# Optimization experiments

Hardware: AMD Instinct MI355X
Metric: run time of the kernel (lower is better)

## Reference

```python
import jax, jax.numpy as jnp
import numpy as np

B, L, D, H, DFF = 4, 2048, 1024, 16, 4096
DH = D // H
INF = 1e12


def setup_inputs() -> dict:
    key = jax.random.key(0)
    ks = jax.random.split(key, 20)
    s = lambda fan_in: 1.0 / np.sqrt(fan_in)
    inp = {
        'x': jax.random.normal(ks[0], (B, L, D), jnp.float32),
        'mask': jax.random.bernoulli(ks[1], 0.1, (B, 1, 1, L)),
        'wq': jax.random.normal(ks[2], (D, D), jnp.float32) * s(D),
        'bq': jnp.zeros((D,), jnp.float32),
        'wk': jax.random.normal(ks[3], (D, D), jnp.float32) * s(D),
        'bk': jnp.zeros((D,), jnp.float32),
        'wv': jax.random.normal(ks[4], (D, D), jnp.float32) * s(D),
        'bv': jnp.zeros((D,), jnp.float32),
        'wo': jax.random.normal(ks[5], (D, D), jnp.float32) * s(D),
        'bo': jnp.zeros((D,), jnp.float32),
        'w1': jax.random.normal(ks[6], (D, DFF), jnp.float32) * s(D),
        'b1': jnp.zeros((DFF,), jnp.float32),
        'w2': jax.random.normal(ks[7], (DFF, D), jnp.float32) * s(DFF),
        'b2': jnp.zeros((D,), jnp.float32),
        'g1': jnp.ones((D,), jnp.float32),
        'beta1': jnp.zeros((D,), jnp.float32),
        'g2': jnp.ones((D,), jnp.float32),
        'beta2': jnp.zeros((D,), jnp.float32),
    }
    return inp


def _layernorm(x, g, b, eps=1e-5):
    mu = jnp.mean(x, axis=-1, keepdims=True)
    var = jnp.mean(jnp.square(x - mu), axis=-1, keepdims=True)
    return (x - mu) * jax.lax.rsqrt(var + eps) * g + b


def reference(x, mask, wq, bq, wk, bk, wv, bv, wo, bo, w1, b1, w2, b2, g1, beta1, g2, beta2):
    # --- self attention ---
    def split_heads(t):  # [B,L,D] -> [B,H,L,DH]
        return t.reshape(B, L, H, DH).transpose(0, 2, 1, 3)

    Q = split_heads(x @ wq + bq)
    K = split_heads(x @ wk + bk)
    V = split_heads(x @ wv + bv)

    dots = jnp.einsum('bhqd,bhkd->bhqk', Q, K) / np.sqrt(DH)  # [B,H,L,L]
    dots = jnp.where(mask, -INF, dots)
    attn = jax.nn.softmax(dots, axis=-1)
    out = jnp.einsum('bhqk,bhkd->bhqd', attn, V)
    out = out.transpose(0, 2, 1, 3).reshape(B, L, D)
    out = out @ wo + bo

    x = _layernorm(x + out, g1, beta1)

    # --- feed forward ---
    h = jax.nn.relu(x @ w1 + b1)
    ff = h @ w2 + b2
    x = _layernorm(x + ff, g2, beta2)
    return x
```

## Files before the change

kernel.cpp:

```cpp
#include <hip/hip_runtime.h>
#include <hip/hip_bf16.h>

#define B_   4
#define L_   2048
#define D_   1024
#define H_   16
#define DH_  64
#define DFF_ 4096
#define M_   (B_ * L_)

typedef __attribute__((ext_vector_type(8))) short bf16x8;
typedef __attribute__((ext_vector_type(4))) float f32x4;

#define GLOAD16(gp, lp)                                                       \
  __builtin_amdgcn_global_load_lds(                                           \
      (const __attribute__((address_space(1))) unsigned int*)(gp),            \
      (__attribute__((address_space(3))) unsigned int*)(lp), 16, 0, 0)

#if __has_builtin(__builtin_amdgcn_exp2f)
#define EXP2F(x) __builtin_amdgcn_exp2f(x)
#else
#define EXP2F(x) exp2f(x)
#endif

__device__ __forceinline__ float bf2f(unsigned short u) {
  return __uint_as_float(((unsigned)u) << 16);
}

__global__ void prep_all(const float4* __restrict__ x4,
                         ushort4* __restrict__ xb4,
                         const unsigned int* __restrict__ mraw,
                         float* __restrict__ maskf,
                         const float* __restrict__ bq,
                         const float* __restrict__ bk,
                         const float* __restrict__ bv,
                         float* __restrict__ biasc) {
  const int id = blockIdx.x;
  if (id < 8192) {
    const int i = id * 256 + threadIdx.x;
    float4 v = x4[i];
    __hip_bfloat16 a = __float2bfloat16(v.x);
    __hip_bfloat16 b = __float2bfloat16(v.y);
    __hip_bfloat16 c = __float2bfloat16(v.z);
    __hip_bfloat16 d = __float2bfloat16(v.w);
    ushort4 o;
    o.x = *reinterpret_cast<unsigned short*>(&a);
    o.y = *reinterpret_cast<unsigned short*>(&b);
    o.z = *reinterpret_cast<unsigned short*>(&c);
    o.w = *reinterpret_cast<unsigned short*>(&d);
    xb4[i] = o;
    return;
  }
  __shared__ int flags[2];
  if (threadIdx.x < 2) flags[threadIdx.x] = 0;
  __syncthreads();
  int nf32 = 0, n01 = 0;
  for (int i = threadIdx.x; i < 2048; i += 256) {
    unsigned w = mraw[i];
    if (w != 0u && w != 0x3f800000u) nf32 = 1;
    if (w > 1u) n01 = 1;
  }
  if (nf32) atomicOr(&flags[0], 1);
  if (n01)  atomicOr(&flags[1], 1);
  __syncthreads();
  const int mode = (!flags[0]) ? 0 : ((!flags[1]) ? 1 : 2);
  const int mi = (id - 8192) * 256 + threadIdx.x;
  if (mi < B_ * L_) {
    bool mk;
    if (mode == 0)      mk = reinterpret_cast<const float*>(mraw)[mi] != 0.f;
    else if (mode == 1) mk = reinterpret_cast<const int*>(mraw)[mi] != 0;
    else                mk = reinterpret_cast<const unsigned char*>(mraw)[mi] != 0;
    maskf[mi] = mk ? -1e12f : -32.0f;
  }
  if (id == 8192) {
#pragma unroll
    for (int j = 0; j < 4; ++j) {
      const int c = j * 256 + threadIdx.x;
      biasc[c] = bq[c];
      biasc[D_ + c] = bk[c];
      biasc[2 * D_ + c] = bv[c];
    }
  }
}

__global__ void transpose_cvt_all(
    const float* __restrict__ wq, const float* __restrict__ wk,
    const float* __restrict__ wv, const float* __restrict__ wo,
    const float* __restrict__ w1, const float* __restrict__ w2,
    __hip_bfloat16* __restrict__ WQT, __hip_bfloat16* __restrict__ WKT,
    __hip_bfloat16* __restrict__ WVT, __hip_bfloat16* __restrict__ WOT,
    __hip_bfloat16* __restrict__ W1T, __hip_bfloat16* __restrict__ W2T) {
  __shared__ float t[32][33];
  const int id = blockIdx.x;
  const float* W;
  __hip_bfloat16* Wt;
  int K, N, rem;
  if (id < 4096) {
    const int which = id >> 10;
    W  = which == 0 ? wq : which == 1 ? wk : which == 2 ? wv : wo;
    Wt = which == 0 ? WQT : which == 1 ? WKT : which == 2 ? WVT : WOT;
    K = D_; N = D_; rem = id & 1023;
  } else if (id < 8192) {
    W = w1; Wt = W1T; K = D_; N = DFF_; rem = id - 4096;
  } else {
    W = w2; Wt = W2T; K = DFF_; N = D_; rem = id - 8192;
  }
  const int ntx = N >> 5;
  const int n0 = (rem % ntx) * 32, k0 = (rem / ntx) * 32;
  const int tx = threadIdx.x, ty = threadIdx.y;
#pragma unroll
  for (int i = 0; i < 4; ++i)
    t[ty + i * 8][tx] = W[(size_t)(k0 + ty + i * 8) * N + n0 + tx];
  __syncthreads();
#pragma unroll
  for (int i = 0; i < 4; ++i)
    Wt[(size_t)(n0 + ty + i * 8) * K + k0 + tx] =
        __float2bfloat16(t[tx][ty + i * 8]);
}

__global__ void transpose_v(const __hip_bfloat16* __restrict__ Vin,
                            __hip_bfloat16* __restrict__ Vt) {
  __shared__ __hip_bfloat16 t[32][33];
  const int l0 = blockIdx.x * 32, d0 = blockIdx.y * 32, b = blockIdx.z;
  const int tx = threadIdx.x, ty = threadIdx.y;
#pragma unroll
  for (int i = 0; i < 4; ++i)
    t[ty + i * 8][tx] = Vin[(size_t)(b * L_ + l0 + ty + i * 8) * D_ + d0 + tx];
  __syncthreads();
#pragma unroll
  for (int i = 0; i < 4; ++i) {
    int d = d0 + ty + i * 8;
    Vt[(size_t)(b * D_ + d) * L_ + l0 + tx] = t[tx][ty + i * 8];
  }
}

#define STAGE8(matptr, stride, ldsbase, tile, kh, rowbase)                    \
  {                                                                           \
    _Pragma("unroll")                                                         \
    for (int j_ = 0; j_ < 2; ++j_) {                                          \
      const int s_ = j_ * 512 + tid;                                          \
      const int row_ = s_ >> 2;                                               \
      const int q_ = (s_ & 3) ^ ((row_ >> 1) & 3);                            \
      GLOAD16(&matptr[(size_t)((rowbase) + row_) * (stride) + (tile) * 64 +   \
                      (kh) * 32 + q_ * 8],                                    \
              (ldsbase) + (j_ * 512 + (w << 6)) * 16);                        \
    }                                                                         \
  }

#define PHASE8(bufoff, rh, ks, dovm, ...)                                     \
  {                                                                           \
    if ((rh) == 0) {                                                          \
      _Pragma("unroll")                                                       \
      for (int j = 0; j < 4; ++j) {                                           \
        const int br = wn * 64 + j * 16 + r16;                                \
        bfr[j] = *reinterpret_cast<const bf16x8*>(                            \
            ldsB + (bufoff) + (ks) * 16384 + br * 64 +                        \
            ((hi * 16) ^ (((br >> 1) & 3) << 4)));                            \
      }                                                                       \
    }                                                                         \
    bf16x8 af[4];                                                             \
    _Pragma("unroll")                                                         \
    for (int i = 0; i < 4; ++i) {                                             \
      const int ar = wm * 128 + (rh) * 64 + i * 16 + r16;                     \
      af[i] = *reinterpret_cast<const bf16x8*>(                               \
          ldsA + (bufoff) + (ks) * 16384 + ar * 64 +                          \
          ((hi * 16) ^ (((ar >> 1) & 3) << 4)));                              \
    }                                                                         \
    __VA_ARGS__;                                                              \
    __builtin_amdgcn_s_barrier();                                             \
    asm volatile("s_waitcnt lgkmcnt(0)" ::: "memory");                        \
    __builtin_amdgcn_sched_barrier(0);                                        \
    __builtin_amdgcn_s_setprio(1);                                            \
    _Pragma("unroll")                                                         \
    for (int i = 0; i < 4; ++i)                                               \
      _Pragma("unroll")                                                       \
      for (int j = 0; j < 4; ++j)                                             \
        acc[(rh) * 4 + i][j] = __builtin_amdgcn_mfma_f32_16x16x32_bf16(       \
            af[i], bfr[j], acc[(rh) * 4 + i][j], 0, 0, 0);                    \
    __builtin_amdgcn_s_setprio(0);                                            \
    if (dovm) {                                                               \
      asm volatile("s_waitcnt vmcnt(4)" ::: "memory");                        \
      __builtin_amdgcn_sched_barrier(0);                                      \
    }                                                                         \
    __builtin_amdgcn_s_barrier();                                             \
  }

template <int EP>
__global__ __launch_bounds__(512, 1) void gemm8(
    const __hip_bfloat16* __restrict__ A, const __hip_bfloat16* __restrict__ Bt,
    const float* __restrict__ bias, void* __restrict__ out,
    int M, int N, int K, int lda, int ldb) {
  __shared__ __align__(16) char lds8[131072];
  char* const ldsA = lds8;
  char* const ldsB = lds8 + 65536;

  const int tid = threadIdx.x;
  const int lane = tid & 63;
  const int w = tid >> 6;
  const int wm = w >> 2;
  const int wn = w & 3;
  const int r16 = lane & 15;
  const int hi = lane >> 4;

  const int nwg = gridDim.x;
  const int orig = blockIdx.x;
  const int swz = (orig & 7) * (nwg >> 3) + (orig >> 3);

  int bm, bn, kh = 0;
  const __hip_bfloat16* Ap = A;
  const __hip_bfloat16* Bp = Bt;
  if (EP == 4) {
    kh = swz & 1;
    const int rest = swz >> 1;
    bm = (rest & 31) * 256;
    bn = (rest >> 5) * 256;
    Ap += (size_t)kh * K;
    Bp += (size_t)kh * K;
  } else {
    bm = (swz & 31) * 256;
    bn = (swz >> 5) * 256;
  }

  f32x4 acc[8][4];
#pragma unroll
  for (int i = 0; i < 8; ++i)
#pragma unroll
    for (int j = 0; j < 4; ++j) acc[i][j] = (f32x4){0.f, 0.f, 0.f, 0.f};
  bf16x8 bfr[4];

  const int nkt = K >> 6;
  const int nit = nkt >> 1;

  STAGE8(Ap, lda, ldsA, 0, 0, bm);
  STAGE8(Bp, ldb, ldsB, 0, 0, bn);
  STAGE8(Ap, lda, ldsA + 16384, 0, 1, bm);
  STAGE8(Bp, ldb, ldsB + 16384, 0, 1, bn);
  STAGE8(Ap, lda, ldsA + 32768, 1, 0, bm);
  STAGE8(Bp, ldb, ldsB + 32768, 1, 0, bn);
  asm volatile("s_waitcnt vmcnt(4)" ::: "memory");
  __builtin_amdgcn_sched_barrier(0);
  __builtin_amdgcn_s_barrier();

  for (int it = 0; it < nit; ++it) {
    const int kt = it * 2;
    const bool hn = (it + 1) < nit;
    PHASE8(0, 0, 0, 0, STAGE8(Ap, lda, ldsA + 49152, kt + 1, 1, bm));
    PHASE8(0, 1, 0, 0, STAGE8(Bp, ldb, ldsB + 49152, kt + 1, 1, bn));
    PHASE8(0, 0, 1, 0, if (hn) STAGE8(Ap, lda, ldsA, kt + 2, 0, bm));
    PHASE8(0, 1, 1, 1, if (hn) STAGE8(Bp, ldb, ldsB, kt + 2, 0, bn));
    PHASE8(32768, 0, 0, 0, if (hn) STAGE8(Ap, lda, ldsA + 16384, kt + 2, 1, bm));
    PHASE8(32768, 1, 0, 0, if (hn) STAGE8(Bp, ldb, ldsB + 16384, kt + 2, 1, bn));
    PHASE8(32768, 0, 1, 0, if (hn) STAGE8(Ap, lda, ldsA + 32768, kt + 3, 0, bm));
    PHASE8(32768, 1, 1, 1, if (hn) STAGE8(Bp, ldb, ldsB + 32768, kt + 3, 0, bn));
  }

#pragma unroll
  for (int ri = 0; ri < 8; ++ri) {
#pragma unroll
    for (int j = 0; j < 4; ++j) {
      const int col = bn + wn * 64 + j * 16 + r16;
      const float bv = (EP == 4) ? 0.f : bias[col];
#pragma unroll
      for (int r = 0; r < 4; ++r) {
        const int row = bm + wm * 128 + ri * 16 + hi * 4 + r;
        const float v = acc[ri][j][r] + bv;
        if (EP == 1) {
          ((__hip_bfloat16*)out)[(size_t)row * N + col] =
              __float2bfloat16(v > 0.f ? v : 0.f);
        } else if (EP == 3) {
          __hip_bfloat16* outp =
              (__hip_bfloat16*)out + (size_t)(col >> 10) * (M_ * D_);
          outp[(size_t)row * 1024 + (col & 1023)] = __float2bfloat16(v);
        } else {
          __hip_bfloat16* outp =
              (__hip_bfloat16*)out + (size_t)kh * ((size_t)M * N);
          outp[(size_t)row * N + col] = __float2bfloat16(v);
        }
      }
    }
  }
}

template <int EP>
__global__ __launch_bounds__(256) void gemm_bt(
    const __hip_bfloat16* __restrict__ A, const __hip_bfloat16* __restrict__ Bt,
    const float* __restrict__ bias, const float* __restrict__ res,
    void* __restrict__ out, int M, int N, int K) {
  __shared__ __align__(16) char As[128 * 64];
  __shared__ __align__(16) char Bs[128 * 64];
  const int tid = threadIdx.x;
  const int lane = tid & 63;
  const int w = tid >> 6;
  const int wm = w >> 1, wn = w & 1;
  const int bm = blockIdx.x * 128;
  const int bn = blockIdx.y * 128;
  const int r16 = lane & 15;
  const int hi = lane >> 4;

  f32x4 acc[4][4];
#pragma unroll
  for (int m = 0; m < 4; ++m)
#pragma unroll
    for (int n = 0; n < 4; ++n) acc[m][n] = (f32x4){0.f, 0.f, 0.f, 0.f};

  for (int k0 = 0; k0 < K; k0 += 32) {
    __syncthreads();
#pragma unroll
    for (int c = 0; c < 2; ++c) {
      const int seg = c * 256 + tid;
      const int row = seg >> 2;
      const int csl = (seg & 3) ^ (row & 3);
      GLOAD16(&A[(size_t)(bm + row) * K + k0 + csl * 8],
              As + (c * 256 + w * 64) * 16);
      GLOAD16(&Bt[(size_t)(bn + row) * K + k0 + csl * 8],
              Bs + (c * 256 + w * 64) * 16);
    }
    __syncthreads();

    bf16x8 af[4], bfr[4];
#pragma unroll
    for (int m = 0; m < 4; ++m) {
      const int arow = wm * 64 + m * 16 + r16;
      af[m] = *reinterpret_cast<const bf16x8*>(
          As + arow * 64 + ((hi * 16) ^ ((arow & 3) << 4)));
    }
#pragma unroll
    for (int n = 0; n < 4; ++n) {
      const int brow = wn * 64 + n * 16 + r16;
      bfr[n] = *reinterpret_cast<const bf16x8*>(
          Bs + brow * 64 + ((hi * 16) ^ ((brow & 3) << 4)));
    }
#pragma unroll
    for (int m = 0; m < 4; ++m)
#pragma unroll
      for (int n = 0; n < 4; ++n)
        acc[m][n] = __builtin_amdgcn_mfma_f32_16x16x32_bf16(af[m], bfr[n],
                                                            acc[m][n], 0, 0, 0);
  }

  const int rg = hi * 4;
#pragma unroll
  for (int m = 0; m < 4; ++m) {
#pragma unroll
    for (int n = 0; n < 4; ++n) {
      const int col = bn + wn * 64 + n * 16 + r16;
      const float bv = bias[col];
#pragma unroll
      for (int r = 0; r < 4; ++r) {
        const int row = bm + wm * 64 + m * 16 + rg + r;
        const size_t idx = (size_t)row * N + col;
        float v = acc[m][n][r] + bv;
        if (EP == 0) {
          ((__hip_bfloat16*)out)[idx] = __float2bfloat16(v);
        } else {
          ((float*)out)[idx] = v + res[idx];
        }
      }
    }
  }
}

__global__ __launch_bounds__(256) void attn_kernel(
    const __hip_bfloat16* __restrict__ Qg, const __hip_bfloat16* __restrict__ Kg,
    const __hip_bfloat16* __restrict__ VTg,
    const float* __restrict__ maskf,
    __hip_bfloat16* __restrict__ Og) {
  __shared__ __align__(16) char Kl[64 * 128];
  __shared__ __align__(16) char Vl[64 * 128];
  __shared__ __align__(16) char Pl[4][32 * 128];
  __shared__ float maskb[64];

  const int tid = threadIdx.x;
  const int lane = tid & 63;
  const int w = tid >> 6;
  const int hi = lane >> 4;
  const int r16 = lane & 15;
  const int swzk = (r16 & 7) << 4;

  const int nwg = gridDim.x;
  const int orig = blockIdx.x;
  const int swb = (orig & 7) * (nwg >> 3) + (orig >> 3);
  const int qb = swb & 15;
  const int bh = swb >> 4;
  const int b = bh >> 4;
  const int h = bh & 15;
  const int qbase = qb * 128 + w * 32;

  const float C = 0.18033688011112042f;
  const short ob = (short)0x3f80;
  const bf16x8 vone = {ob, ob, ob, ob, ob, ob, ob, ob};

  bf16x8 qf[2][2];
#pragma unroll
  for (int m = 0; m < 2; ++m)
#pragma unroll
    for (int ks = 0; ks < 2; ++ks)
      qf[m][ks] = *reinterpret_cast<const bf16x8*>(
          &Qg[(size_t)(b * L_ + qbase + m * 16 + r16) * D_ + h * DH_ +
              ks * 32 + hi * 8]);

  f32x4 o[2][4];
  f32x4 oden[2];
#pragma unroll
  for (int m = 0; m < 2; ++m) {
    oden[m] = (f32x4){0.f, 0.f, 0.f, 0.f};
#pragma unroll
    for (int nd = 0; nd < 4; ++nd) o[m][nd] = (f32x4){0.f, 0.f, 0.f, 0.f};
  }

  char* const Plw = Pl[w];

  for (int kv0 = 0; kv0 < L_; kv0 += 64) {
    __syncthreads();
#pragma unroll
    for (int c = 0; c < 2; ++c) {
      const int seg = c * 256 + tid;
      const int row = seg >> 3;
      const int csl = (seg & 7) ^ (row & 7);
      GLOAD16(&Kg[(size_t)(b * L_ + kv0 + row) * D_ + h * DH_ + csl * 8],
              Kl + (c * 256 + w * 64) * 16);
      GLOAD16(&VTg[(size_t)(b * D_ + h * DH_ + row) * L_ + kv0 + csl * 8],
              Vl + (c * 256 + w * 64) * 16);
    }
    if (tid < 64) maskb[tid] = maskf[(size_t)b * L_ + kv0 + tid];
    __syncthreads();

    f32x4 sacc[2][4];
#pragma unroll
    for (int m = 0; m < 2; ++m)
#pragma unroll
      for (int n = 0; n < 4; ++n) sacc[m][n] = (f32x4){0.f, 0.f, 0.f, 0.f};
    __builtin_amdgcn_s_setprio(1);
#pragma unroll
    for (int n = 0; n < 4; ++n) {
      const int krow = n * 16 + r16;
#pragma unroll
      for (int ks = 0; ks < 2; ++ks) {
        const bf16x8 kf = *reinterpret_cast<const bf16x8*>(
            Kl + krow * 128 + ((ks * 64 + hi * 16) ^ swzk));
#pragma unroll
        for (int m = 0; m < 2; ++m)
          sacc[m][n] = __builtin_amdgcn_mfma_f32_16x16x32_bf16(
              kf, qf[m][ks], sacc[m][n], 0, 0, 0);
      }
    }
    __builtin_amdgcn_s_setprio(0);

    float4 mv[4];
#pragma unroll
    for (int n = 0; n < 4; ++n)
      mv[n] = *reinterpret_cast<const float4*>(&maskb[n * 16 + hi * 4]);
#pragma unroll
    for (int m = 0; m < 2; ++m) {
      const int prow = m * 16 + r16;
#pragma unroll
      for (int n = 0; n < 4; ++n) {
        const float e0 = EXP2F(fmaf(sacc[m][n][0], C, mv[n].x));
        const float e1 = EXP2F(fmaf(sacc[m][n][1], C, mv[n].y));
        const float e2 = EXP2F(fmaf(sacc[m][n][2], C, mv[n].z));
        const float e3 = EXP2F(fmaf(sacc[m][n][3], C, mv[n].w));
        union { unsigned long long u; unsigned short us[4]; } pk;
        __hip_bfloat16 t0 = __float2bfloat16(e0);
        __hip_bfloat16 t1 = __float2bfloat16(e1);
        __hip_bfloat16 t2 = __float2bfloat16(e2);
        __hip_bfloat16 t3 = __float2bfloat16(e3);
        pk.us[0] = *reinterpret_cast<unsigned short*>(&t0);
        pk.us[1] = *reinterpret_cast<unsigned short*>(&t1);
        pk.us[2] = *reinterpret_cast<unsigned short*>(&t2);
        pk.us[3] = *reinterpret_cast<unsigned short*>(&t3);
        *reinterpret_cast<unsigned long long*>(
            Plw + prow * 128 + ((n * 32 + hi * 8) ^ swzk)) = pk.u;
      }
    }

    bf16x8 pa[2][2];
#pragma unroll
    for (int m = 0; m < 2; ++m)
#pragma unroll
      for (int ks = 0; ks < 2; ++ks)
        pa[m][ks] = *reinterpret_cast<const bf16x8*>(
            Plw + (m * 16 + r16) * 128 + ((ks * 64 + hi * 16) ^ swzk));
    __builtin_amdgcn_s_setprio(1);
#pragma unroll
    for (int m = 0; m < 2; ++m)
#pragma unroll
      for (int ks = 0; ks < 2; ++ks)
        oden[m] = __builtin_amdgcn_mfma_f32_16x16x32_bf16(pa[m][ks], vone,
                                                          oden[m], 0, 0, 0);
#pragma unroll
    for (int nd = 0; nd < 4; ++nd) {
      const int vrow = nd * 16 + r16;
#pragma unroll
      for (int ks = 0; ks < 2; ++ks) {
        const bf16x8 vb = *reinterpret_cast<const bf16x8*>(
            Vl + vrow * 128 + ((ks * 64 + hi * 16) ^ swzk));
#pragma unroll
        for (int m = 0; m < 2; ++m)
          o[m][nd] = __builtin_amdgcn_mfma_f32_16x16x32_bf16(pa[m][ks], vb,
                                                             o[m][nd], 0, 0, 0);
      }
    }
    __builtin_amdgcn_s_setprio(0);
  }

#pragma unroll
  for (int m = 0; m < 2; ++m) {
#pragma unroll
    for (int r = 0; r < 4; ++r) {
      const float ir = 1.f / oden[m][r];
      const int q = qbase + m * 16 + hi * 4 + r;
#pragma unroll
      for (int nd = 0; nd < 4; ++nd)
        Og[(size_t)(b * L_ + q) * D_ + h * DH_ + nd * 16 + r16] =
            __float2bfloat16(o[m][nd][r] * ir);
    }
  }
}

__global__ __launch_bounds__(256) void layernorm_kernel(
    const float* __restrict__ in, const float* __restrict__ g,
    const float* __restrict__ be, float* __restrict__ outf,
    __hip_bfloat16* __restrict__ outb) {
  const int row = blockIdx.x;
  const int tid = threadIdx.x;
  const float4 v = reinterpret_cast<const float4*>(in + (size_t)row * D_)[tid];
  float s = v.x + v.y + v.z + v.w;
  float ss = v.x * v.x + v.y * v.y + v.z * v.z + v.w * v.w;
#pragma unroll
  for (int off = 1; off < 64; off <<= 1) {
    s += __shfl_xor(s, off, 64);
    ss += __shfl_xor(ss, off, 64);
  }
  __shared__ float red[8];
  const int w = tid >> 6, lane = tid & 63;
  if (lane == 0) { red[w] = s; red[4 + w] = ss; }
  __syncthreads();
  s = red[0] + red[1] + red[2] + red[3];
  ss = red[4] + red[5] + red[6] + red[7];
  const float mu = s * (1.f / D_);
  const float rs = rsqrtf(ss * (1.f / D_) - mu * mu + 1e-5f);
  const float4 gv = reinterpret_cast<const float4*>(g)[tid];
  const float4 bv = reinterpret_cast<const float4*>(be)[tid];
  float4 ov;
  ov.x = (v.x - mu) * rs * gv.x + bv.x;
  ov.y = (v.y - mu) * rs * gv.y + bv.y;
  ov.z = (v.z - mu) * rs * gv.z + bv.z;
  ov.w = (v.w - mu) * rs * gv.w + bv.w;
  reinterpret_cast<float4*>(outf + (size_t)row * D_)[tid] = ov;
  if (outb) {
    __hip_bfloat16 t[4] = {__float2bfloat16(ov.x), __float2bfloat16(ov.y),
                           __float2bfloat16(ov.z), __float2bfloat16(ov.w)};
    *reinterpret_cast<uint2*>(&outb[(size_t)row * D_ + tid * 4]) =
        *reinterpret_cast<const uint2*>(t);
  }
}

__global__ __launch_bounds__(256) void ln_addres(
    const __hip_bfloat16* __restrict__ OP, const float* __restrict__ x,
    const float* __restrict__ g, const float* __restrict__ be,
    float* __restrict__ outf, __hip_bfloat16* __restrict__ outb) {
  const int row = blockIdx.x;
  const int tid = threadIdx.x;
  const ushort4 a4 = reinterpret_cast<const ushort4*>(OP + (size_t)row * D_)[tid];
  const float4 xr = reinterpret_cast<const float4*>(x + (size_t)row * D_)[tid];
  float4 v;
  v.x = bf2f(a4.x) + xr.x;
  v.y = bf2f(a4.y) + xr.y;
  v.z = bf2f(a4.z) + xr.z;
  v.w = bf2f(a4.w) + xr.w;
  float s = v.x + v.y + v.z + v.w;
  float ss = v.x * v.x + v.y * v.y + v.z * v.z + v.w * v.w;
#pragma unroll
  for (int off = 1; off < 64; off <<= 1) {
    s += __shfl_xor(s, off, 64);
    ss += __shfl_xor(ss, off, 64);
  }
  __shared__ float red[8];
  const int w = tid >> 6, lane = tid & 63;
  if (lane == 0) { red[w] = s; red[4 + w] = ss; }
  __syncthreads();
  s = red[0] + red[1] + red[2] + red[3];
  ss = red[4] + red[5] + red[6] + red[7];
  const float mu = s * (1.f / D_);
  const float rs = rsqrtf(ss * (1.f / D_) - mu * mu + 1e-5f);
  const float4 gv = reinterpret_cast<const float4*>(g)[tid];
  const float4 bv = reinterpret_cast<const float4*>(be)[tid];
  float4 ov;
  ov.x = (v.x - mu) * rs * gv.x + bv.x;
  ov.y = (v.y - mu) * rs * gv.y + bv.y;
  ov.z = (v.z - mu) * rs * gv.z + bv.z;
  ov.w = (v.w - mu) * rs * gv.w + bv.w;
  reinterpret_cast<float4*>(outf + (size_t)row * D_)[tid] = ov;
  __hip_bfloat16 t[4] = {__float2bfloat16(ov.x), __float2bfloat16(ov.y),
                         __float2bfloat16(ov.z), __float2bfloat16(ov.w)};
  *reinterpret_cast<uint2*>(&outb[(size_t)row * D_ + tid * 4]) =
      *reinterpret_cast<const uint2*>(t);
}

__global__ __launch_bounds__(256) void ln_addres_sk(
    const __hip_bfloat16* __restrict__ P0, const __hip_bfloat16* __restrict__ P1,
    const float* __restrict__ x, const float* __restrict__ bo,
    const float* __restrict__ g, const float* __restrict__ be,
    float* __restrict__ outf, __hip_bfloat16* __restrict__ outb) {
  const int row = blockIdx.x;
  const int tid = threadIdx.x;
  const ushort4 a4 = reinterpret_cast<const ushort4*>(P0 + (size_t)row * D_)[tid];
  const ushort4 b4 = reinterpret_cast<const ushort4*>(P1 + (size_t)row * D_)[tid];
  const float4 xr = reinterpret_cast<const float4*>(x + (size_t)row * D_)[tid];
  const float4 bb = reinterpret_cast<const float4*>(bo)[tid];
  float4 v;
  v.x = bf2f(a4.x) + bf2f(b4.x) + xr.x + bb.x;
  v.y = bf2f(a4.y) + bf2f(b4.y) + xr.y + bb.y;
  v.z = bf2f(a4.z) + bf2f(b4.z) + xr.z + bb.z;
  v.w = bf2f(a4.w) + bf2f(b4.w) + xr.w + bb.w;
  float s = v.x + v.y + v.z + v.w;
  float ss = v.x * v.x + v.y * v.y + v.z * v.z + v.w * v.w;
#pragma unroll
  for (int off = 1; off < 64; off <<= 1) {
    s += __shfl_xor(s, off, 64);
    ss += __shfl_xor(ss, off, 64);
  }
  __shared__ float red[8];
  const int w = tid >> 6, lane = tid & 63;
  if (lane == 0) { red[w] = s; red[4 + w] = ss; }
  __syncthreads();
  s = red[0] + red[1] + red[2] + red[3];
  ss = red[4] + red[5] + red[6] + red[7];
  const float mu = s * (1.f / D_);
  const float rs = rsqrtf(ss * (1.f / D_) - mu * mu + 1e-5f);
  const float4 gv = reinterpret_cast<const float4*>(g)[tid];
  const float4 bv = reinterpret_cast<const float4*>(be)[tid];
  float4 ov;
  ov.x = (v.x - mu) * rs * gv.x + bv.x;
  ov.y = (v.y - mu) * rs * gv.y + bv.y;
  ov.z = (v.z - mu) * rs * gv.z + bv.z;
  ov.w = (v.w - mu) * rs * gv.w + bv.w;
  reinterpret_cast<float4*>(outf + (size_t)row * D_)[tid] = ov;
  __hip_bfloat16 t[4] = {__float2bfloat16(ov.x), __float2bfloat16(ov.y),
                         __float2bfloat16(ov.z), __float2bfloat16(ov.w)};
  *reinterpret_cast<uint2*>(&outb[(size_t)row * D_ + tid * 4]) =
      *reinterpret_cast<const uint2*>(t);
}

__global__ __launch_bounds__(256) void combine_ln2(
    const __hip_bfloat16* __restrict__ P0, const __hip_bfloat16* __restrict__ P1,
    const float* __restrict__ res, const float* __restrict__ b2,
    const float* __restrict__ g, const float* __restrict__ be,
    float* __restrict__ out) {
  const int row = blockIdx.x;
  const int tid = threadIdx.x;
  const ushort4 a4 =
      reinterpret_cast<const ushort4*>(P0 + (size_t)row * D_)[tid];
  const ushort4 b4 =
      reinterpret_cast<const ushort4*>(P1 + (size_t)row * D_)[tid];
  const float4 rr = reinterpret_cast<const float4*>(res + (size_t)row * D_)[tid];
  const float4 bb = reinterpret_cast<const float4*>(b2)[tid];
  float4 v;
  v.x = bf2f(a4.x) + bf2f(b4.x) + rr.x + bb.x;
  v.y = bf2f(a4.y) + bf2f(b4.y) + rr.y + bb.y;
  v.z = bf2f(a4.z) + bf2f(b4.z) + rr.z + bb.z;
  v.w = bf2f(a4.w) + bf2f(b4.w) + rr.w + bb.w;
  float s = v.x + v.y + v.z + v.w;
  float ss = v.x * v.x + v.y * v.y + v.z * v.z + v.w * v.w;
#pragma unroll
  for (int off = 1; off < 64; off <<= 1) {
    s += __shfl_xor(s, off, 64);
    ss += __shfl_xor(ss, off, 64);
  }
  __shared__ float red[8];
  const int w = tid >> 6, lane = tid & 63;
  if (lane == 0) { red[w] = s; red[4 + w] = ss; }
  __syncthreads();
  s = red[0] + red[1] + red[2] + red[3];
  ss = red[4] + red[5] + red[6] + red[7];
  const float mu = s * (1.f / D_);
  const float rs = rsqrtf(ss * (1.f / D_) - mu * mu + 1e-5f);
  const float4 gv = reinterpret_cast<const float4*>(g)[tid];
  const float4 bv = reinterpret_cast<const float4*>(be)[tid];
  float4 ov;
  ov.x = (v.x - mu) * rs * gv.x + bv.x;
  ov.y = (v.y - mu) * rs * gv.y + bv.y;
  ov.z = (v.z - mu) * rs * gv.z + bv.z;
  ov.w = (v.w - mu) * rs * gv.w + bv.w;
  reinterpret_cast<float4*>(out + (size_t)row * D_)[tid] = ov;
}

extern "C" void kernel_launch(void* const* d_in, const int* in_sizes, int n_in,
                              void* d_out, int out_size, void* d_ws,
                              size_t ws_size, hipStream_t stream) {
  (void)in_sizes; (void)n_in; (void)out_size;
  const float* x   = (const float*)d_in[0];
  const void*  msk = d_in[1];
  const float* wq  = (const float*)d_in[2];
  const float* bq  = (const float*)d_in[3];
  const float* wk  = (const float*)d_in[4];
  const float* bk  = (const float*)d_in[5];
  const float* wv  = (const float*)d_in[6];
  const float* bv  = (const float*)d_in[7];
  const float* wo  = (const float*)d_in[8];
  const float* bo  = (const float*)d_in[9];
  const float* w1  = (const float*)d_in[10];
  const float* b1  = (const float*)d_in[11];
  const float* w2  = (const float*)d_in[12];
  const float* b2  = (const float*)d_in[13];
  const float* g1  = (const float*)d_in[14];
  const float* be1 = (const float*)d_in[15];
  const float* g2  = (const float*)d_in[16];
  const float* be2 = (const float*)d_in[17];

  char* ws = (char*)d_ws;
  float*          MASKF = (float*)(ws + 256);
  float*          BIASC = (float*)(ws + 40960);
  __hip_bfloat16* XB    = (__hip_bfloat16*)(ws + 65536);
  __hip_bfloat16* WQT   = (__hip_bfloat16*)(ws + 16842752);
  __hip_bfloat16* WKT   = (__hip_bfloat16*)(ws + 18939904);
  __hip_bfloat16* WVT   = (__hip_bfloat16*)(ws + 21037056);
  __hip_bfloat16* WOT   = (__hip_bfloat16*)(ws + 23134208);
  __hip_bfloat16* W1T   = (__hip_bfloat16*)(ws + 25231360);
  __hip_bfloat16* W2T   = (__hip_bfloat16*)(ws + 33619968);
  __hip_bfloat16* QB    = (__hip_bfloat16*)(ws + 42008576);
  __hip_bfloat16* KB    = (__hip_bfloat16*)(ws + 58785792);
  __hip_bfloat16* VB    = (__hip_bfloat16*)(ws + 75563008);
  __hip_bfloat16* OB    = (__hip_bfloat16*)(ws + 92340224);
  __hip_bfloat16* HB    = QB;
  __hip_bfloat16* VT    = (__hip_bfloat16*)(ws + 109117440);
  __hip_bfloat16* OP    = VT;
  float*          R1    = (float*)(ws + 125894656);
  __hip_bfloat16* P0    = (__hip_bfloat16*)(ws + 159449088);
  __hip_bfloat16* P1    = (__hip_bfloat16*)(ws + 176226304);
  float*          OUT   = (float*)d_out;
  const bool use_splitk = ws_size >= 193003520ull;

  prep_all<<<8224, 256, 0, stream>>>((const float4*)x, (ushort4*)XB,
                                     (const unsigned int*)msk, MASKF,
                                     bq, bk, bv, BIASC);
  transpose_cvt_all<<<12288, dim3(32, 8), 0, stream>>>(
      wq, wk, wv, wo, w1, w2, WQT, WKT, WVT, WOT, W1T, W2T);

  gemm8<3><<<dim3((M_ / 256) * (3 * D_ / 256)), 512, 0, stream>>>(
      XB, WQT, BIASC, QB, M_, 3 * D_, D_, D_, D_);

  transpose_v<<<dim3(L_ / 32, D_ / 32, B_), dim3(32, 8), 0, stream>>>(VB, VT);
  attn_kernel<<<dim3(B_ * H_ * (L_ / 128)), 256, 0, stream>>>(QB, KB, VT, MASKF, OB);

  if (use_splitk) {
    gemm8<4><<<dim3((M_ / 256) * (D_ / 256) * 2), 512, 0, stream>>>(
        OB, WOT, nullptr, P0, M_, D_, D_ / 2, D_, D_);
    ln_addres_sk<<<M_, 256, 0, stream>>>(P0, P1, x, bo, g1, be1, R1, XB);
  } else {
    gemm_bt<0><<<dim3(M_ / 128, D_ / 128), 256, 0, stream>>>(OB, WOT, bo, nullptr, OP, M_, D_, D_);
    ln_addres<<<M_, 256, 0, stream>>>(OP, x, g1, be1, R1, XB);
  }

  gemm8<1><<<dim3((M_ / 256) * (DFF_ / 256)), 512, 0, stream>>>(
      XB, W1T, b1, HB, M_, DFF_, D_, D_, D_);
  if (use_splitk) {
    gemm8<4><<<dim3((M_ / 256) * (D_ / 256) * 2), 512, 0, stream>>>(
        HB, W2T, nullptr, P0, M_, D_, DFF_ / 2, DFF_, DFF_);
    combine_ln2<<<M_, 256, 0, stream>>>(P0, P1, R1, b2, g2, be2, OUT);
  } else {
    gemm_bt<2><<<dim3(M_ / 128, D_ / 128), 256, 0, stream>>>(HB, W2T, b2, R1, OUT, M_, D_, DFF_);
    layernorm_kernel<<<M_, 256, 0, stream>>>(OUT, g2, be2, OUT, nullptr);
  }
}
```

Before: 416.8 us.

## Load K/V fragments directly from global memory instead of staging in LDS

The attention kernel no longer copies K, V^T and the mask tile into shared memory each KV step. Each wave now reads its MFMA operand fragments straight from global memory, relying on L1/L2 caches for reuse across the four waves. This removes the two block-wide barriers per iteration and the LDS staging traffic, and also drops the s_setprio hints. The cost is four times more global/L2 requests for K and V, since each wave fetches the same tile, and the loads are no longer swizzled or asynchronous.

Result: slower. 629.9 us (+51.1%).

```diff
diff --git a/kernel.cpp b/kernel.cpp
--- a/kernel.cpp
+++ b/kernel.cpp
@@ -365,10 +365,7 @@
     const __hip_bfloat16* __restrict__ VTg,
     const float* __restrict__ maskf,
     __hip_bfloat16* __restrict__ Og) {
-  __shared__ __align__(16) char Kl[64 * 128];
-  __shared__ __align__(16) char Vl[64 * 128];
   __shared__ __align__(16) char Pl[4][32 * 128];
-  __shared__ float maskb[64];
 
   const int tid = threadIdx.x;
   const int lane = tid & 63;
@@ -390,6 +387,10 @@
   const short ob = (short)0x3f80;
   const bf16x8 vone = {ob, ob, ob, ob, ob, ob, ob, ob};
 
+  const __hip_bfloat16* const Kb = Kg + (size_t)(b * L_) * D_ + h * DH_;
+  const __hip_bfloat16* const Vb = VTg + (size_t)(b * D_ + h * DH_) * L_;
+  const float* const mb = maskf + (size_t)b * L_;
+
   bf16x8 qf[2][2];
 #pragma unroll
   for (int m = 0; m < 2; ++m)
@@ -411,45 +412,29 @@
   char* const Plw = Pl[w];
 
   for (int kv0 = 0; kv0 < L_; kv0 += 64) {
-    __syncthreads();
-#pragma unroll
-    for (int c = 0; c < 2; ++c) {
-      const int seg = c * 256 + tid;
-      const int row = seg >> 3;
-      const int csl = (seg & 7) ^ (row & 7);
-      GLOAD16(&Kg[(size_t)(b * L_ + kv0 + row) * D_ + h * DH_ + csl * 8],
-              Kl + (c * 256 + w * 64) * 16);
-      GLOAD16(&VTg[(size_t)(b * D_ + h * DH_ + row) * L_ + kv0 + csl * 8],
-              Vl + (c * 256 + w * 64) * 16);
-    }
-    if (tid < 64) maskb[tid] = maskf[(size_t)b * L_ + kv0 + tid];
-    __syncthreads();
-
     f32x4 sacc[2][4];
 #pragma unroll
     for (int m = 0; m < 2; ++m)
 #pragma unroll
       for (int n = 0; n < 4; ++n) sacc[m][n] = (f32x4){0.f, 0.f, 0.f, 0.f};
-    __builtin_amdgcn_s_setprio(1);
 #pragma unroll
     for (int n = 0; n < 4; ++n) {
-      const int krow = n * 16 + r16;
+      const size_t krow = (size_t)(kv0 + n * 16 + r16) * D_;
 #pragma unroll
       for (int ks = 0; ks < 2; ++ks) {
-        const bf16x8 kf = *reinterpret_cast<const bf16x8*>(
-            Kl + krow * 128 + ((ks * 64 + hi * 16) ^ swzk));
+        const bf16x8 kf =
+            *reinterpret_cast<const bf16x8*>(Kb + krow + ks * 32 + hi * 8);
 #pragma unroll
         for (int m = 0; m < 2; ++m)
           sacc[m][n] = __builtin_amdgcn_mfma_f32_16x16x32_bf16(
               kf, qf[m][ks], sacc[m][n], 0, 0, 0);
       }
     }
-    __builtin_amdgcn_s_setprio(0);
 
     float4 mv[4];
 #pragma unroll
     for (int n = 0; n < 4; ++n)
-      mv[n] = *reinterpret_cast<const float4*>(&maskb[n * 16 + hi * 4]);
+      mv[n] = *reinterpret_cast<const float4*>(mb + kv0 + n * 16 + hi * 4);
 #pragma unroll
     for (int m = 0; m < 2; ++m) {
       const int prow = m * 16 + r16;
@@ -480,7 +465,6 @@
       for (int ks = 0; ks < 2; ++ks)
         pa[m][ks] = *reinterpret_cast<const bf16x8*>(
             Plw + (m * 16 + r16) * 128 + ((ks * 64 + hi * 16) ^ swzk));
-    __builtin_amdgcn_s_setprio(1);
 #pragma unroll
     for (int m = 0; m < 2; ++m)
 #pragma unroll
@@ -489,18 +473,17 @@
                                                           oden[m], 0, 0, 0);
 #pragma unroll
     for (int nd = 0; nd < 4; ++nd) {
-      const int vrow = nd * 16 + r16;
+      const size_t vrow = (size_t)(nd * 16 + r16) * L_;
 #pragma unroll
       for (int ks = 0; ks < 2; ++ks) {
         const bf16x8 vb = *reinterpret_cast<const bf16x8*>(
-            Vl + vrow * 128 + ((ks * 64 + hi * 16) ^ swzk));
+            Vb + vrow + kv0 + ks * 32 + hi * 8);
 #pragma unroll
         for (int m = 0; m < 2; ++m)
           o[m][nd] = __builtin_amdgcn_mfma_f32_16x16x32_bf16(pa[m][ks], vb,
                                                              o[m][nd], 0, 0, 0);
       }
     }
-    __builtin_amdgcn_s_setprio(0);
   }
 
 #pragma unroll
```
